# Kernel tuning notes

Hardware: AMD Instinct MI355X
Metric: run time of the kernel (lower is better)

Reference implementation:

```python
import jax, jax.numpy as jnp
import numpy as np

B, L, H = 16, 2048, 768
INNER = max(H // 2, 32)
RADIUS = 2
K_STEPS = 4
ETA = 0.1
ETA_DECAY = 0.9
MU_MAX = 10.0
LAM = 0.1


def _window_edges(length, radius):
    ei, ej = [], []
    for r in range(1, radius + 1):
        i = np.arange(length - r)
        ei.append(i)
        ej.append(i + r)
    return (jnp.asarray(np.concatenate(ei), jnp.int32),
            jnp.asarray(np.concatenate(ej), jnp.int32))


def setup_inputs() -> dict:
    key = jax.random.key(0)
    ks = jax.random.split(key, 6)
    hidden = jax.random.normal(ks[0], (B, L, H), jnp.float32)
    attention_mask = jnp.ones((B, L), jnp.int32)  # uniform full lengths -> single bucket, window path
    w1 = jax.random.normal(ks[1], (2, INNER), jnp.float32) * 0.2
    b1 = jnp.zeros((INNER,), jnp.float32)
    w2 = jax.random.normal(ks[2], (INNER, 1), jnp.float32) * 0.05
    b2 = jnp.zeros((1,), jnp.float32)
    wq = jax.random.normal(ks[3], (H, H), jnp.float32) * (1.0 / np.sqrt(H))
    bq = jnp.zeros((H,), jnp.float32)
    gamma = jnp.ones((H,), jnp.float32)
    beta = jnp.zeros((H,), jnp.float32)
    edges_i, edges_j = _window_edges(L, RADIUS)
    return dict(hidden=hidden, attention_mask=attention_mask, w1=w1, b1=b1,
                w2=w2, b2=b2, wq=wq, bq=bq, gamma=gamma, beta=beta,
                edges_i=edges_i, edges_j=edges_j)


def _friction(hidden, w1, b1, w2, b2, wq, bq, gamma, beta, edges_i, edges_j):
    eps = 1e-6
    q = hidden @ wq + bq                      # [B,L,H]
    state = hidden
    mu = None
    for step in range(K_STEPS):
        # edge weights from current state (recompute_mu=True)
        h_i = state[:, edges_i]               # [B,E,H] gather
        h_j = state[:, edges_j]
        diff = h_i - h_j
        dist = jnp.sqrt(jnp.sum(diff * diff, -1))
        n_i = jnp.maximum(jnp.sqrt(jnp.sum(h_i * h_i, -1)), eps)
        n_j = jnp.maximum(jnp.sqrt(jnp.sum(h_j * h_j, -1)), eps)
        cos = jnp.sum(h_i * h_j, -1) / (n_i * n_j)
        feats = jnp.stack([dist, cos], -1)    # [B,E,2]
        mid = jax.nn.gelu(feats @ w1 + b1, approximate=False)
        mu = jnp.minimum(jax.nn.softplus((mid @ w2 + b2)[..., 0]) + 1e-5, MU_MAX)  # [B,E]
        # normalized weighted graph Laplacian applied to state
        w = mu[..., None] * diff
        deg = jnp.zeros((state.shape[0], state.shape[1]), state.dtype)
        deg = deg.at[:, edges_i].add(mu).at[:, edges_j].add(mu)
        inv = jnp.maximum(deg, 1e-6) ** -0.5
        w = w * (inv[:, edges_i] * inv[:, edges_j])[..., None]
        lap = jnp.zeros_like(state).at[:, edges_i].add(w).at[:, edges_j].add(-w)
        state = state - (ETA * ETA_DECAY ** step) * (lap - q)
        # 1D chain smoothing with replicated boundaries
        left = jnp.concatenate([state[:, :1], state[:, :-1]], 1)
        right = jnp.concatenate([state[:, 1:], state[:, -1:]], 1)
        state = state - LAM * (2 * state - left - right)
    # edge energy with last mu and final state: 0.5 * sum_e mu_e ||s_i - s_j||^2
    df = state[:, edges_i] - state[:, edges_j]
    energy = 0.5 * jnp.sum(mu * jnp.sum(df * df, -1), axis=1)  # [B]
    res = state + hidden
    mean = jnp.mean(res, -1, keepdims=True)
    var = jnp.mean((res - mean) ** 2, -1, keepdims=True)
    out = (res - mean) / jnp.sqrt(var + 1e-5) * gamma + beta
    return out, energy


def reference(hidden, attention_mask, w1, b1, w2, b2, wq, bq, gamma, beta, edges_i, edges_j):
    # all masks are full-length ones -> single bucket, batched window path
    return _friction(hidden, w1, b1, w2, b2, wq, bq, gamma, beta, edges_i, edges_j)
```

## Files before the change

### kernel.cpp

```cpp
#include <hip/hip_runtime.h>
#include <hip/hip_bf16.h>
#include <math.h>

#define B_ 16
#define L_ 2048
#define H_ 768
#define INNER_ 384
#define MU_MAX_ 10.0f
#define LAM_ 0.1f
#define EDGES_ (2 * L_ - 3)

typedef short v8bf __attribute__((ext_vector_type(8)));
typedef float v4f  __attribute__((ext_vector_type(4)));

static __device__ __forceinline__ float wave_sum(float v) {
    #pragma unroll
    for (int o = 32; o > 0; o >>= 1) v += __shfl_xor(v, o, 64);
    return v;
}

static __device__ __forceinline__ float dot4(const float4& a, const float4& b) {
    return a.x * b.x + a.y * b.y + a.z * b.z + a.w * b.w;
}

static __device__ __forceinline__ void fma4(float4& a, float c, float4 x) {
    a.x = fmaf(c, x.x, a.x); a.y = fmaf(c, x.y, a.y);
    a.z = fmaf(c, x.z, a.z); a.w = fmaf(c, x.w, a.w);
}

static __device__ __forceinline__ ushort f2bf(float x) {
    unsigned u = __float_as_uint(x);
    u += 0x7fffu + ((u >> 16) & 1u);
    return (ushort)(u >> 16);
}

__global__ __launch_bounds__(256) void conv_bf16_kernel(
    const float* __restrict__ in, ushort* __restrict__ out, int n8)
{
    int t = blockIdx.x * 256 + threadIdx.x;
    if (t >= n8) return;
    float4 a = ((const float4*)in)[2 * t];
    float4 b = ((const float4*)in)[2 * t + 1];
    ushort r[8] = { f2bf(a.x), f2bf(a.y), f2bf(a.z), f2bf(a.w),
                    f2bf(b.x), f2bf(b.y), f2bf(b.z), f2bf(b.w) };
    ((v8bf*)out)[t] = *(v8bf*)r;
}

__global__ __launch_bounds__(256) void conv_wqt_kernel(
    const float* __restrict__ wq, ushort* __restrict__ wt)
{
    __shared__ float tile[64][65];
    int k0 = blockIdx.x * 64, n0 = blockIdx.y * 64;
    int t = threadIdx.x;
    #pragma unroll
    for (int it = 0; it < 16; ++it) {
        int lin = t + it * 256;
        int r = lin >> 6, c = lin & 63;
        tile[r][c] = wq[(size_t)(k0 + r) * H_ + n0 + c];
    }
    __syncthreads();
    #pragma unroll
    for (int it = 0; it < 16; ++it) {
        int lin = t + it * 256;
        int r = lin >> 6, c = lin & 63;
        wt[(size_t)(n0 + r) * H_ + k0 + c] = f2bf(tile[c][r]);
    }
}

#define GBM 128
#define GBN 128
#define GBK 64
#define LSTR 72

__global__ __launch_bounds__(256) void gemm_q_kernel(
    const ushort* __restrict__ A, const ushort* __restrict__ Wt,
    const float* __restrict__ bias, float* __restrict__ C)
{
    __shared__ ushort As[GBM * LSTR];
    __shared__ ushort Bs[GBN * LSTR];
    const int K = H_, N = H_;
    int m0 = blockIdx.x * GBM;
    int n0 = blockIdx.y * GBN;
    int t = threadIdx.x;
    int lane = t & 63, w = t >> 6;
    int wm = (w & 1) * 64, wn = (w >> 1) * 64;
    int row16 = lane & 15, quad = lane >> 4;

    v4f acc[4][4];
    #pragma unroll
    for (int i = 0; i < 4; ++i)
        #pragma unroll
        for (int j = 0; j < 4; ++j)
            acc[i][j] = (v4f){0.f, 0.f, 0.f, 0.f};

    for (int k0 = 0; k0 < K; k0 += GBK) {
        #pragma unroll
        for (int it = 0; it < 4; ++it) {
            int lin = t + it * 256;
            int r = lin >> 3;
            int s = lin & 7;
            *(v8bf*)&As[r * LSTR + s * 8] =
                *(const v8bf*)(A + (size_t)(m0 + r) * K + k0 + s * 8);
            *(v8bf*)&Bs[r * LSTR + s * 8] =
                *(const v8bf*)(Wt + (size_t)(n0 + r) * K + k0 + s * 8);
        }
        __syncthreads();
        #pragma unroll
        for (int h = 0; h < 2; ++h) {
            v8bf af[4], bf[4];
            #pragma unroll
            for (int i = 0; i < 4; ++i)
                af[i] = *(v8bf*)&As[(wm + i * 16 + row16) * LSTR + h * 32 + quad * 8];
            #pragma unroll
            for (int j = 0; j < 4; ++j)
                bf[j] = *(v8bf*)&Bs[(wn + j * 16 + row16) * LSTR + h * 32 + quad * 8];
            #pragma unroll
            for (int i = 0; i < 4; ++i)
                #pragma unroll
                for (int j = 0; j < 4; ++j)
                    acc[i][j] = __builtin_amdgcn_mfma_f32_16x16x32_bf16(
                        af[i], bf[j], acc[i][j], 0, 0, 0);
        }
        __syncthreads();
    }
    #pragma unroll
    for (int j = 0; j < 4; ++j) {
        int ncol = n0 + wn + j * 16 + row16;
        float bqv = bias[ncol];
        #pragma unroll
        for (int i = 0; i < 4; ++i) {
            int mrow = m0 + wm + i * 16 + quad * 4;
            #pragma unroll
            for (int r = 0; r < 4; ++r)
                C[(size_t)(mrow + r) * N + ncol] = acc[i][j][r] + bqv;
        }
    }
}

static __device__ __forceinline__ float mu_mlp2(
    float si, float sj, float dotij,
    const float* w1d, const float* w1c, const float* b1v, const float* w2v,
    float b2v)
{
    float dist = sqrtf(fmaxf(si + sj - 2.f * dotij, 0.f));
    float cosv = dotij / (fmaxf(sqrtf(si), 1e-6f) * fmaxf(sqrtf(sj), 1e-6f));
    float acc = 0.f;
    #pragma unroll
    for (int k = 0; k < 6; ++k) {
        float z = fmaf(dist, w1d[k], fmaf(cosv, w1c[k], b1v[k]));
        float g = 0.5f * z * (1.f + erff(z * 0.70710678118654752f));
        acc = fmaf(g, w2v[k], acc);
    }
    acc = wave_sum(acc) + b2v;
    float sp = fmaxf(acc, 0.f) + log1pf(expf(-fabsf(acc)));
    return fminf(sp + 1e-5f, MU_MAX_);
}

__global__ __launch_bounds__(256) void mu_kernel(
    const float* __restrict__ src,
    const float* __restrict__ w1, const float* __restrict__ b1,
    const float* __restrict__ w2, const float* __restrict__ b2,
    float* __restrict__ mu)
{
    int blk = blockIdx.x;
    int sw = (blk & 7) * ((B_ * L_ / 4) / 8) + (blk >> 3);
    int rg = sw * 4 + (threadIdx.x >> 6);
    int lane = threadIdx.x & 63;
    int b = rg >> 11;
    int t = rg & (L_ - 1);
    int o1 = (t + 1 < L_) ? 1 : 0;
    int o2 = (t + 2 < L_) ? 2 : (L_ - 1 - t);
    const float4* r0p = (const float4*)(src + (size_t)rg * H_);
    const float4* r1p = (const float4*)(src + (size_t)(rg + o1) * H_);
    const float4* r2p = (const float4*)(src + (size_t)(rg + o2) * H_);
    float ss0 = 0.f, ss1 = 0.f, ss2 = 0.f, d1 = 0.f, d2 = 0.f;
    #pragma unroll
    for (int ch = 0; ch < 3; ++ch) {
        int off = ch * 64 + lane;
        float4 x = r0p[off], y = r1p[off], z = r2p[off];
        ss0 += dot4(x, x); ss1 += dot4(y, y); ss2 += dot4(z, z);
        d1  += dot4(x, y); d2  += dot4(x, z);
    }
    if (t >= L_ - 1) return;
    ss0 = wave_sum(ss0); ss1 = wave_sum(ss1); d1 = wave_sum(d1);

    float w1d[6], w1c[6], b1v[6], w2v[6];
    #pragma unroll
    for (int k = 0; k < 6; ++k) {
        int u = k * 64 + lane;
        w1d[k] = w1[u]; w1c[k] = w1[INNER_ + u]; b1v[k] = b1[u]; w2v[k] = w2[u];
    }
    float b2v = b2[0];

    float m1 = mu_mlp2(ss0, ss1, d1, w1d, w1c, b1v, w2v, b2v);
    if (lane == 0) mu[(size_t)b * EDGES_ + t] = m1;
    if (t < L_ - 2) {
        ss2 = wave_sum(ss2); d2 = wave_sum(d2);
        float m2v = mu_mlp2(ss0, ss2, d2, w1d, w1c, b1v, w2v, b2v);
        if (lane == 0) mu[(size_t)b * EDGES_ + (L_ - 1) + t] = m2v;
    }
}

__global__ __launch_bounds__(256) void update_kernel(
    const float* __restrict__ src, const float* __restrict__ q,
    const float* __restrict__ mu, float* __restrict__ dst,
    const float* __restrict__ hidden, const float* __restrict__ gamma,
    const float* __restrict__ beta, float* __restrict__ lnout,
    float coef)
{
    int blk = blockIdx.x;
    int sw = (blk & 7) * ((B_ * L_ / 4) / 8) + (blk >> 3);
    int rg = sw * 4 + (threadIdx.x >> 6);
    int lane = threadIdx.x & 63;
    int b = rg >> 11;
    int p = rg & (L_ - 1);
    const float* mp = mu + (size_t)b * EDGES_;

    float m1a[8];
    #pragma unroll
    for (int j = 0; j < 8; ++j) {
        int u = p - 4 + j;
        m1a[j] = (u >= 0 && u < L_ - 1) ? mp[u] : 0.f;
    }
    float m2a[9];
    #pragma unroll
    for (int j = 0; j < 9; ++j) {
        int u = p - 5 + j;
        m2a[j] = (u >= 0 && u < L_ - 2) ? mp[(L_ - 1) + u] : 0.f;
    }
    float invv[7];
    #pragma unroll
    for (int d = 0; d < 7; ++d) {
        int u = p - 3 + d;
        if (u < 0 || u >= L_) { invv[d] = 0.f; }
        else {
            float deg = m1a[d + 1] + m1a[d] + m2a[d + 2] + m2a[d];
            invv[d] = 1.f / sqrtf(fmaxf(deg, 1e-6f));
        }
    }
    float gwv[3];
    gwv[0] = (p == 0) ? 0.f : LAM_;
    gwv[2] = (p == L_ - 1) ? 0.f : LAM_;
    gwv[1] = 1.f - 2.f * LAM_ + ((p == 0 || p == L_ - 1) ? LAM_ : 0.f);

    float C[7] = {0.f, 0.f, 0.f, 0.f, 0.f, 0.f, 0.f};
    float e[3];
    #pragma unroll
    for (int i = 0; i < 3; ++i) {
        float g = gwv[i];
        float wm2 = m2a[i + 2] * invv[i + 2] * invv[i];
        float wm1 = m1a[i + 2] * invv[i + 2] * invv[i + 1];
        float wp1 = m1a[i + 3] * invv[i + 2] * invv[i + 3];
        float wp2 = m2a[i + 4] * invv[i + 2] * invv[i + 4];
        float wsum = wm2 + wm1 + wp1 + wp2;
        C[i]     = fmaf(g * coef, wm2, C[i]);
        C[i + 1] = fmaf(g * coef, wm1, C[i + 1]);
        C[i + 2] = fmaf(g, fmaf(-coef, wsum, 1.f), C[i + 2]);
        C[i + 3] = fmaf(g * coef, wp1, C[i + 3]);
        C[i + 4] = fmaf(g * coef, wp2, C[i + 4]);
        e[i] = g * coef;
    }

    int rr[7];
    #pragma unroll
    for (int d = 0; d < 7; ++d) {
        int u = p - 3 + d;
        rr[d] = u < 0 ? 0 : (u >= L_ ? L_ - 1 : u);
    }
    int qr[3];
    #pragma unroll
    for (int i = 0; i < 3; ++i) {
        int u = p - 1 + i;
        qr[i] = u < 0 ? 0 : (u >= L_ ? L_ - 1 : u);
    }
    const float* sB = src + (size_t)b * L_ * H_;
    const float* qB = q + (size_t)b * L_ * H_;
    float4 res[3];
    #pragma unroll
    for (int ch = 0; ch < 3; ++ch) {
        int off = ch * 64 + lane;
        float4 acc = {0.f, 0.f, 0.f, 0.f};
        #pragma unroll
        for (int d = 0; d < 7; ++d)
            fma4(acc, C[d], ((const float4*)(sB + (size_t)rr[d] * H_))[off]);
        #pragma unroll
        for (int i = 0; i < 3; ++i)
            fma4(acc, e[i], ((const float4*)(qB + (size_t)qr[i] * H_))[off]);
        ((float4*)(dst + (size_t)rg * H_))[off] = acc;
        res[ch] = acc;
    }

    if (lnout) {
        const float4* hB = (const float4*)(hidden + (size_t)rg * H_);
        float sum = 0.f, sq = 0.f;
        float4 r[3];
        #pragma unroll
        for (int ch = 0; ch < 3; ++ch) {
            int off = ch * 64 + lane;
            float4 h = hB[off];
            float4 v;
            v.x = res[ch].x + h.x; v.y = res[ch].y + h.y;
            v.z = res[ch].z + h.z; v.w = res[ch].w + h.w;
            r[ch] = v;
            sum += v.x + v.y + v.z + v.w;
            sq  += v.x * v.x + v.y * v.y + v.z * v.z + v.w * v.w;
        }
        sum = wave_sum(sum); sq = wave_sum(sq);
        float mean = sum * (1.f / H_);
        float var  = sq * (1.f / H_) - mean * mean;
        float rs = 1.f / sqrtf(var + 1e-5f);
        #pragma unroll
        for (int ch = 0; ch < 3; ++ch) {
            int off = ch * 64 + lane;
            float4 g4 = ((const float4*)gamma)[off];
            float4 b4 = ((const float4*)beta)[off];
            float4 o;
            o.x = (r[ch].x - mean) * rs * g4.x + b4.x;
            o.y = (r[ch].y - mean) * rs * g4.y + b4.y;
            o.z = (r[ch].z - mean) * rs * g4.z + b4.z;
            o.w = (r[ch].w - mean) * rs * g4.w + b4.w;
            ((float4*)(lnout + (size_t)rg * H_))[off] = o;
        }
    }
}

__global__ void zero_energy_kernel(float* __restrict__ e) {
    if (threadIdx.x < B_) e[threadIdx.x] = 0.f;
}

#define EPW 16
__global__ __launch_bounds__(256) void energy_kernel(
    const float* __restrict__ state, const int* __restrict__ ei, const int* __restrict__ ej,
    const float* __restrict__ mu, float* __restrict__ energy, int E)
{
    __shared__ float red[4];
    int wib = threadIdx.x >> 6;
    int lane = threadIdx.x & 63;
    int nchunk = (E + 63) / 64;
    int b = blockIdx.x / nchunk;
    int chunk = blockIdx.x - b * nchunk;
    int e0 = chunk * 64 + wib * EPW;
    const float* base = state + (size_t)b * L_ * H_;
    const float* muB = mu + (size_t)b * E;
    float part = 0.f;
    for (int k = 0; k < EPW; ++k) {
        int e = e0 + k;
        if (e >= E) break;
        int i = ei[e], j = ej[e];
        const float4* ri = (const float4*)(base + (size_t)i * H_);
        const float4* rj = (const float4*)(base + (size_t)j * H_);
        float s = 0.f;
        #pragma unroll
        for (int it = 0; it < 3; ++it) {
            float4 xi = ri[it * 64 + lane], xj = rj[it * 64 + lane];
            float dx = xi.x - xj.x, dy = xi.y - xj.y, dz = xi.z - xj.z, dw = xi.w - xj.w;
            s += dx*dx + dy*dy + dz*dz + dw*dw;
        }
        s = wave_sum(s);
        part += muB[e] * s;
    }
    if (lane == 0) red[wib] = part;
    __syncthreads();
    if (threadIdx.x == 0)
        atomicAdd(energy + b, 0.5f * (red[0] + red[1] + red[2] + red[3]));
}

extern "C" void kernel_launch(void* const* d_in, const int* in_sizes, int n_in,
                              void* d_out, int out_size, void* d_ws, size_t ws_size,
                              hipStream_t stream)
{
    const float* hidden = (const float*)d_in[0];
    const float* w1 = (const float*)d_in[2];
    const float* b1 = (const float*)d_in[3];
    const float* w2 = (const float*)d_in[4];
    const float* b2 = (const float*)d_in[5];
    const float* wq = (const float*)d_in[6];
    const float* bq = (const float*)d_in[7];
    const float* gamma = (const float*)d_in[8];
    const float* beta  = (const float*)d_in[9];
    const int* ei = (const int*)d_in[10];
    const int* ej = (const int*)d_in[11];
    int E = in_sizes[10];

    const size_t BLH = (size_t)B_ * L_ * H_;
    float* out = (float*)d_out;
    float* energy = out + BLH;

    float* q    = (float*)d_ws;
    float* bufA = q + BLH;
    float* bufB = bufA + BLH;
    float* mu   = bufB + BLH;
    ushort* Abf = (ushort*)bufA;
    ushort* wt  = (ushort*)(mu + (size_t)B_ * E);

    int n8 = (int)(BLH / 8);
    conv_bf16_kernel<<<(n8 + 255) / 256, 256, 0, stream>>>(hidden, Abf, n8);
    conv_wqt_kernel<<<dim3(H_ / 64, H_ / 64), 256, 0, stream>>>(wq, wt);
    gemm_q_kernel<<<dim3((B_ * L_) / GBM, H_ / GBN), 256, 0, stream>>>(Abf, wt, bq, q);
    zero_energy_kernel<<<1, 64, 0, stream>>>(energy);

    const int NB = B_ * L_ / 4;
    float coef = 0.1f;
    const float* st = hidden;
    float* dsts[4] = {bufA, bufB, bufA, bufB};
    for (int s = 0; s < 4; ++s) {
        mu_kernel<<<NB, 256, 0, stream>>>(st, w1, b1, w2, b2, mu);
        float* lno = (s == 3) ? out : nullptr;
        update_kernel<<<NB, 256, 0, stream>>>(st, q, mu, dsts[s],
                                              hidden, gamma, beta, lno, coef);
        st = dsts[s];
        coef *= 0.9f;
    }

    int nchunk = (E + 63) / 64;
    energy_kernel<<<B_ * nchunk, 256, 0, stream>>>(bufB, ei, ej, mu, energy, E);
}
```

Baseline: 803.1 us.

## Fuse edge-statistics into update kernel and fold bf16 conversion into GEMM

Drops the separate fp32-to-bf16 pass over hidden by converting inside the GEMM tile load. The update kernel now handles 8 rows per block with an extra halo wave. It stages the new rows in shared memory and emits per-row squared norms and neighbour dot products, so the next step's mu only needs a light MLP kernel instead of re-reading the full state. Each wave computes two rows while sharing neighbour loads, which cuts redundant global traffic, at the cost of a 30KB shared buffer and a 320-thread block shape.

```diff
diff --git a/kernel.cpp b/kernel.cpp
--- a/kernel.cpp
+++ b/kernel.cpp
@@ -34,18 +34,6 @@
     return (ushort)(u >> 16);
 }
 
-__global__ __launch_bounds__(256) void conv_bf16_kernel(
-    const float* __restrict__ in, ushort* __restrict__ out, int n8)
-{
-    int t = blockIdx.x * 256 + threadIdx.x;
-    if (t >= n8) return;
-    float4 a = ((const float4*)in)[2 * t];
-    float4 b = ((const float4*)in)[2 * t + 1];
-    ushort r[8] = { f2bf(a.x), f2bf(a.y), f2bf(a.z), f2bf(a.w),
-                    f2bf(b.x), f2bf(b.y), f2bf(b.z), f2bf(b.w) };
-    ((v8bf*)out)[t] = *(v8bf*)r;
-}
-
 __global__ __launch_bounds__(256) void conv_wqt_kernel(
     const float* __restrict__ wq, ushort* __restrict__ wt)
 {
@@ -73,7 +61,7 @@
 #define LSTR 72
 
 __global__ __launch_bounds__(256) void gemm_q_kernel(
-    const ushort* __restrict__ A, const ushort* __restrict__ Wt,
+    const float* __restrict__ A32, const ushort* __restrict__ Wt,
     const float* __restrict__ bias, float* __restrict__ C)
 {
     __shared__ ushort As[GBM * LSTR];
@@ -99,8 +87,12 @@
             int lin = t + it * 256;
             int r = lin >> 3;
             int s = lin & 7;
-            *(v8bf*)&As[r * LSTR + s * 8] =
-                *(const v8bf*)(A + (size_t)(m0 + r) * K + k0 + s * 8);
+            const float* ap = A32 + (size_t)(m0 + r) * K + k0 + s * 8;
+            float4 f0 = *(const float4*)ap;
+            float4 f1 = *(const float4*)(ap + 4);
+            ushort tmp[8] = { f2bf(f0.x), f2bf(f0.y), f2bf(f0.z), f2bf(f0.w),
+                              f2bf(f1.x), f2bf(f1.y), f2bf(f1.z), f2bf(f1.w) };
+            *(v8bf*)&As[r * LSTR + s * 8] = *(v8bf*)tmp;
             *(v8bf*)&Bs[r * LSTR + s * 8] =
                 *(const v8bf*)(Wt + (size_t)(n0 + r) * K + k0 + s * 8);
         }
@@ -201,21 +193,39 @@
     }
 }
 
-__global__ __launch_bounds__(256) void update_kernel(
-    const float* __restrict__ src, const float* __restrict__ q,
-    const float* __restrict__ mu, float* __restrict__ dst,
-    const float* __restrict__ hidden, const float* __restrict__ gamma,
-    const float* __restrict__ beta, float* __restrict__ lnout,
-    float coef)
-{
-    int blk = blockIdx.x;
-    int sw = (blk & 7) * ((B_ * L_ / 4) / 8) + (blk >> 3);
-    int rg = sw * 4 + (threadIdx.x >> 6);
+__global__ __launch_bounds__(256) void mu_mlp_kernel(
+    const float* __restrict__ ssS, const float* __restrict__ d1S,
+    const float* __restrict__ d2S,
+    const float* __restrict__ w1, const float* __restrict__ b1,
+    const float* __restrict__ w2, const float* __restrict__ b2,
+    float* __restrict__ mu)
+{
+    int rg = blockIdx.x * 4 + (threadIdx.x >> 6);
     int lane = threadIdx.x & 63;
     int b = rg >> 11;
-    int p = rg & (L_ - 1);
-    const float* mp = mu + (size_t)b * EDGES_;
-
+    int t = rg & (L_ - 1);
+    if (t >= L_ - 1) return;
+    size_t base = (size_t)b * L_;
+    float ss0 = ssS[base + t], ss1 = ssS[base + t + 1], d1 = d1S[base + t];
+    float w1d[6], w1c[6], b1v[6], w2v[6];
+    #pragma unroll
+    for (int k = 0; k < 6; ++k) {
+        int u = k * 64 + lane;
+        w1d[k] = w1[u]; w1c[k] = w1[INNER_ + u]; b1v[k] = b1[u]; w2v[k] = w2[u];
+    }
+    float b2v = b2[0];
+    float m1 = mu_mlp2(ss0, ss1, d1, w1d, w1c, b1v, w2v, b2v);
+    if (lane == 0) mu[(size_t)b * EDGES_ + t] = m1;
+    if (t < L_ - 2) {
+        float ss2 = ssS[base + t + 2], d2 = d2S[base + t];
+        float m2v = mu_mlp2(ss0, ss2, d2, w1d, w1c, b1v, w2v, b2v);
+        if (lane == 0) mu[(size_t)b * EDGES_ + (L_ - 1) + t] = m2v;
+    }
+}
+
+static __device__ __forceinline__ void row_coeffs(
+    int p, const float* __restrict__ mp, float coef, float C[7], float e[3])
+{
     float m1a[8];
     #pragma unroll
     for (int j = 0; j < 8; ++j) {
@@ -242,9 +252,8 @@
     gwv[0] = (p == 0) ? 0.f : LAM_;
     gwv[2] = (p == L_ - 1) ? 0.f : LAM_;
     gwv[1] = 1.f - 2.f * LAM_ + ((p == 0 || p == L_ - 1) ? LAM_ : 0.f);
-
-    float C[7] = {0.f, 0.f, 0.f, 0.f, 0.f, 0.f, 0.f};
-    float e[3];
+    #pragma unroll
+    for (int d = 0; d < 7; ++d) C[d] = 0.f;
     #pragma unroll
     for (int i = 0; i < 3; ++i) {
         float g = gwv[i];
@@ -260,66 +269,146 @@
         C[i + 4] = fmaf(g * coef, wp2, C[i + 4]);
         e[i] = g * coef;
     }
-
-    int rr[7];
-    #pragma unroll
-    for (int d = 0; d < 7; ++d) {
-        int u = p - 3 + d;
-        rr[d] = u < 0 ? 0 : (u >= L_ ? L_ - 1 : u);
-    }
-    int qr[3];
-    #pragma unroll
-    for (int i = 0; i < 3; ++i) {
-        int u = p - 1 + i;
-        qr[i] = u < 0 ? 0 : (u >= L_ ? L_ - 1 : u);
-    }
+}
+
+static __device__ __forceinline__ void ln_store(
+    const float4 rr[3], const float* __restrict__ hrow,
+    const float* __restrict__ gamma, const float* __restrict__ beta,
+    float* __restrict__ orow, int lane)
+{
+    float sum = 0.f, sq = 0.f;
+    float4 v[3];
+    #pragma unroll
+    for (int ch = 0; ch < 3; ++ch) {
+        int off = ch * 64 + lane;
+        float4 h = ((const float4*)hrow)[off];
+        float4 x = rr[ch];
+        x.x += h.x; x.y += h.y; x.z += h.z; x.w += h.w;
+        v[ch] = x;
+        sum += x.x + x.y + x.z + x.w;
+        sq  += x.x * x.x + x.y * x.y + x.z * x.z + x.w * x.w;
+    }
+    sum = wave_sum(sum); sq = wave_sum(sq);
+    float mean = sum * (1.f / H_);
+    float var  = sq * (1.f / H_) - mean * mean;
+    float rs = 1.f / sqrtf(var + 1e-5f);
+    #pragma unroll
+    for (int ch = 0; ch < 3; ++ch) {
+        int off = ch * 64 + lane;
+        float4 g4 = ((const float4*)gamma)[off];
+        float4 b4 = ((const float4*)beta)[off];
+        float4 o;
+        o.x = (v[ch].x - mean) * rs * g4.x + b4.x;
+        o.y = (v[ch].y - mean) * rs * g4.y + b4.y;
+        o.z = (v[ch].z - mean) * rs * g4.z + b4.z;
+        o.w = (v[ch].w - mean) * rs * g4.w + b4.w;
+        ((float4*)orow)[off] = o;
+    }
+}
+
+template <int EMIT, int LN>
+__global__ __launch_bounds__(320, 5) void upd_fused_kernel(
+    const float* __restrict__ src, const float* __restrict__ q,
+    const float* __restrict__ mu, float* __restrict__ dst,
+    float* __restrict__ ssS, float* __restrict__ d1S, float* __restrict__ d2S,
+    const float* __restrict__ hidden, const float* __restrict__ gamma,
+    const float* __restrict__ beta, float* __restrict__ lnout, float coef)
+{
+    __shared__ float rows[10][H_];
+    int blk = blockIdx.x;
+    int chunk = (blk & 7) * ((B_ * L_ / 8) / 8) + (blk >> 3);
+    int b = chunk >> 8;
+    int p0 = (chunk & 255) * 8;
+    int w = threadIdx.x >> 6, lane = threadIdx.x & 63;
+
+    if (!EMIT && w == 4) return;
+
+    const float* mp = mu + (size_t)b * EDGES_;
     const float* sB = src + (size_t)b * L_ * H_;
     const float* qB = q + (size_t)b * L_ * H_;
-    float4 res[3];
+
+    int ta = p0 + 2 * w;
+    int tac = min(ta, L_ - 1);
+    int tbc = min(ta + 1, L_ - 1);
+
+    float CA[7], eA[3], CB[7], eB[3];
+    row_coeffs(tac, mp, coef, CA, eA);
+    row_coeffs(tbc, mp, coef, CB, eB);
+
+    const float* sp[8];
+    #pragma unroll
+    for (int u = 0; u < 8; ++u) {
+        int g = min(max(tac - 3 + u, 0), L_ - 1);
+        sp[u] = sB + (size_t)g * H_;
+    }
+    const float* qp[4];
+    #pragma unroll
+    for (int u = 0; u < 4; ++u) {
+        int g = min(max(tac - 1 + u, 0), L_ - 1);
+        qp[u] = qB + (size_t)g * H_;
+    }
+
+    float4 keepA[3], keepB[3];
     #pragma unroll
     for (int ch = 0; ch < 3; ++ch) {
         int off = ch * 64 + lane;
-        float4 acc = {0.f, 0.f, 0.f, 0.f};
-        #pragma unroll
-        for (int d = 0; d < 7; ++d)
-            fma4(acc, C[d], ((const float4*)(sB + (size_t)rr[d] * H_))[off]);
-        #pragma unroll
-        for (int i = 0; i < 3; ++i)
-            fma4(acc, e[i], ((const float4*)(qB + (size_t)qr[i] * H_))[off]);
-        ((float4*)(dst + (size_t)rg * H_))[off] = acc;
-        res[ch] = acc;
-    }
-
-    if (lnout) {
-        const float4* hB = (const float4*)(hidden + (size_t)rg * H_);
-        float sum = 0.f, sq = 0.f;
-        float4 r[3];
-        #pragma unroll
-        for (int ch = 0; ch < 3; ++ch) {
-            int off = ch * 64 + lane;
-            float4 h = hB[off];
-            float4 v;
-            v.x = res[ch].x + h.x; v.y = res[ch].y + h.y;
-            v.z = res[ch].z + h.z; v.w = res[ch].w + h.w;
-            r[ch] = v;
-            sum += v.x + v.y + v.z + v.w;
-            sq  += v.x * v.x + v.y * v.y + v.z * v.z + v.w * v.w;
-        }
-        sum = wave_sum(sum); sq = wave_sum(sq);
-        float mean = sum * (1.f / H_);
-        float var  = sq * (1.f / H_) - mean * mean;
-        float rs = 1.f / sqrtf(var + 1e-5f);
-        #pragma unroll
-        for (int ch = 0; ch < 3; ++ch) {
-            int off = ch * 64 + lane;
-            float4 g4 = ((const float4*)gamma)[off];
-            float4 b4 = ((const float4*)beta)[off];
-            float4 o;
-            o.x = (r[ch].x - mean) * rs * g4.x + b4.x;
-            o.y = (r[ch].y - mean) * rs * g4.y + b4.y;
-            o.z = (r[ch].z - mean) * rs * g4.z + b4.z;
-            o.w = (r[ch].w - mean) * rs * g4.w + b4.w;
-            ((float4*)(lnout + (size_t)rg * H_))[off] = o;
+        float4 S[8], Q[4];
+        #pragma unroll
+        for (int u = 0; u < 8; ++u) S[u] = ((const float4*)sp[u])[off];
+        #pragma unroll
+        for (int u = 0; u < 4; ++u) Q[u] = ((const float4*)qp[u])[off];
+        float4 a = {0.f, 0.f, 0.f, 0.f}, c2 = {0.f, 0.f, 0.f, 0.f};
+        #pragma unroll
+        for (int d = 0; d < 7; ++d) { fma4(a, CA[d], S[d]); fma4(c2, CB[d], S[d + 1]); }
+        #pragma unroll
+        for (int i = 0; i < 3; ++i) { fma4(a, eA[i], Q[i]); fma4(c2, eB[i], Q[i + 1]); }
+        if (EMIT) {
+            ((float4*)rows[2 * w])[off] = a;
+            ((float4*)rows[2 * w + 1])[off] = c2;
+        }
+        if (w < 4) {
+            ((float4*)(dst + ((size_t)b * L_ + ta) * H_))[off] = a;
+            ((float4*)(dst + ((size_t)b * L_ + ta + 1) * H_))[off] = c2;
+        }
+        if (LN) { keepA[ch] = a; keepB[ch] = c2; }
+    }
+
+    if (LN && w < 4) {
+        size_t rowA = (size_t)b * L_ + ta;
+        ln_store(keepA, hidden + rowA * H_, gamma, beta, lnout + rowA * H_, lane);
+        ln_store(keepB, hidden + (rowA + 1) * H_, gamma, beta,
+                 lnout + (rowA + 1) * H_, lane);
+    }
+
+    if (EMIT) {
+        __syncthreads();
+        if (w < 4) {
+            int r0 = 2 * w;
+            float s0 = 0.f, s1 = 0.f, ea = 0.f, eb = 0.f, ec = 0.f, ed = 0.f;
+            #pragma unroll
+            for (int ch = 0; ch < 3; ++ch) {
+                int off = ch * 64 + lane;
+                float4 x0 = ((const float4*)rows[r0])[off];
+                float4 x1 = ((const float4*)rows[r0 + 1])[off];
+                float4 x2 = ((const float4*)rows[r0 + 2])[off];
+                float4 x3 = ((const float4*)rows[r0 + 3])[off];
+                s0 += dot4(x0, x0); s1 += dot4(x1, x1);
+                ea += dot4(x0, x1); eb += dot4(x1, x2);
+                ec += dot4(x0, x2); ed += dot4(x1, x3);
+            }
+            s0 = wave_sum(s0); s1 = wave_sum(s1);
+            ea = wave_sum(ea); eb = wave_sum(eb);
+            ec = wave_sum(ec); ed = wave_sum(ed);
+            if (lane == 0) {
+                size_t base = (size_t)b * L_;
+                int t0 = p0 + r0, t1 = t0 + 1;
+                ssS[base + t0] = s0;
+                ssS[base + t1] = s1;
+                if (t0 < L_ - 1) d1S[base + t0] = ea;
+                if (t1 < L_ - 1) d1S[base + t1] = eb;
+                if (t0 < L_ - 2) d2S[base + t0] = ec;
+                if (t1 < L_ - 2) d2S[base + t1] = ed;
+            }
         }
     }
 }
@@ -390,27 +479,35 @@
     float* bufA = q + BLH;
     float* bufB = bufA + BLH;
     float* mu   = bufB + BLH;
-    ushort* Abf = (ushort*)bufA;
-    ushort* wt  = (ushort*)(mu + (size_t)B_ * E);
-
-    int n8 = (int)(BLH / 8);
-    conv_bf16_kernel<<<(n8 + 255) / 256, 256, 0, stream>>>(hidden, Abf, n8);
+    ushort* wt  = (ushort*)(mu + (size_t)B_ * EDGES_);
+    float* ssS  = (float*)(wt + (size_t)H_ * H_);
+    float* d1S  = ssS + (size_t)B_ * L_;
+    float* d2S  = d1S + (size_t)B_ * L_;
+
     conv_wqt_kernel<<<dim3(H_ / 64, H_ / 64), 256, 0, stream>>>(wq, wt);
-    gemm_q_kernel<<<dim3((B_ * L_) / GBM, H_ / GBN), 256, 0, stream>>>(Abf, wt, bq, q);
+    gemm_q_kernel<<<dim3((B_ * L_) / GBM, H_ / GBN), 256, 0, stream>>>(hidden, wt, bq, q);
     zero_energy_kernel<<<1, 64, 0, stream>>>(energy);
 
-    const int NB = B_ * L_ / 4;
+    mu_kernel<<<B_ * L_ / 4, 256, 0, stream>>>(hidden, w1, b1, w2, b2, mu);
+
+    const int NBU = B_ * L_ / 8;
+    const int NBM = B_ * L_ / 4;
     float coef = 0.1f;
-    const float* st = hidden;
-    float* dsts[4] = {bufA, bufB, bufA, bufB};
-    for (int s = 0; s < 4; ++s) {
-        mu_kernel<<<NB, 256, 0, stream>>>(st, w1, b1, w2, b2, mu);
-        float* lno = (s == 3) ? out : nullptr;
-        update_kernel<<<NB, 256, 0, stream>>>(st, q, mu, dsts[s],
-                                              hidden, gamma, beta, lno, coef);
-        st = dsts[s];
-        coef *= 0.9f;
-    }
+
+    upd_fused_kernel<1, 0><<<NBU, 320, 0, stream>>>(hidden, q, mu, bufA,
+        ssS, d1S, d2S, hidden, gamma, beta, nullptr, coef);
+    mu_mlp_kernel<<<NBM, 256, 0, stream>>>(ssS, d1S, d2S, w1, b1, w2, b2, mu);
+    coef *= 0.9f;
+    upd_fused_kernel<1, 0><<<NBU, 320, 0, stream>>>(bufA, q, mu, bufB,
+        ssS, d1S, d2S, hidden, gamma, beta, nullptr, coef);
+    mu_mlp_kernel<<<NBM, 256, 0, stream>>>(ssS, d1S, d2S, w1, b1, w2, b2, mu);
+    coef *= 0.9f;
+    upd_fused_kernel<1, 0><<<NBU, 320, 0, stream>>>(bufB, q, mu, bufA,
+        ssS, d1S, d2S, hidden, gamma, beta, nullptr, coef);
+    mu_mlp_kernel<<<NBM, 256, 0, stream>>>(ssS, d1S, d2S, w1, b1, w2, b2, mu);
+    coef *= 0.9f;
+    upd_fused_kernel<0, 1><<<NBU, 320, 0, stream>>>(bufA, q, mu, bufB,
+        ssS, d1S, d2S, hidden, gamma, beta, out, coef);
 
     int nchunk = (E + 63) / 64;
     energy_kernel<<<B_ * nchunk, 256, 0, stream>>>(bufB, ei, ej, mu, energy, E);
```

Measured after the change: 992.9 us. 1.24x slower.
